# Optimization experiments

Hardware: AMD Instinct MI355X
Metric: run time of the kernel (lower is better)

Reference implementation:

```python
import jax, jax.numpy as jnp
import numpy as np

N = 50000      # ncount
IN_CH = 256    # in_channels
OUT_CH = 128   # out_channels
NNZ = 800000   # nnz per sparse matrix (avg degree 16)


def _spmm(rows, cols, vals, dense, n_rows):
    # sparse(COO) @ dense : gather rows of dense by col index, scale, scatter-add by row
    contrib = vals[:, None] * dense[cols]              # [nnz, F]
    return jax.ops.segment_sum(contrib, rows, num_segments=n_rows)


def setup_inputs() -> dict:
    key = jax.random.key(0)
    ks = jax.random.split(key, 12)
    phi_indices = jnp.stack([
        jax.random.randint(ks[0], (NNZ,), 0, N),
        jax.random.randint(ks[1], (NNZ,), 0, N)])
    phi_values = jax.random.normal(ks[2], (NNZ,), dtype=jnp.float32)
    phi_inverse_indices = jnp.stack([
        jax.random.randint(ks[3], (NNZ,), 0, N),
        jax.random.randint(ks[4], (NNZ,), 0, N)])
    phi_inverse_values = jax.random.normal(ks[5], (NNZ,), dtype=jnp.float32)
    feature_indices = jnp.stack([
        jax.random.randint(ks[6], (NNZ,), 0, N),       # node index
        jax.random.randint(ks[7], (NNZ,), 0, IN_CH)])  # feature column
    feature_values = jax.random.normal(ks[8], (NNZ,), dtype=jnp.float32)
    # xavier_uniform for weight_matrix
    limit = float(np.sqrt(6.0 / (IN_CH + OUT_CH)))
    weight_matrix = jax.random.uniform(ks[9], (IN_CH, OUT_CH), jnp.float32, -limit, limit)
    # diagonal filter Theta init uniform(0.9, 1.1)
    diagonal_weight_filter = jax.random.uniform(ks[10], (N,), jnp.float32, 0.9, 1.1)
    return {
        "phi_indices": phi_indices,
        "phi_values": phi_values,
        "phi_inverse_indices": phi_inverse_indices,
        "phi_inverse_values": phi_inverse_values,
        "feature_indices": feature_indices,
        "feature_values": feature_values,
        "weight_matrix": weight_matrix,
        "diagonal_weight_filter": diagonal_weight_filter,
        "dropout": 0,
    }


def reference(phi_indices, phi_values, phi_inverse_indices, phi_inverse_values,
              feature_indices, feature_values, weight_matrix,
              diagonal_weight_filter, dropout):
    # rescaled_phi = phi @ diag(theta): scales column j of phi by theta[j]
    scaled_phi_vals = phi_values * diagonal_weight_filter[phi_indices[1]]
    # filtered = features(sparse N x IN) @ W  -> [N, OUT]
    filtered = _spmm(feature_indices[0], feature_indices[1], feature_values,
                     weight_matrix, N)
    # (phi * D * phi_inv) @ filtered computed associatively without dense N x N:
    tmp = _spmm(phi_inverse_indices[0], phi_inverse_indices[1],
                phi_inverse_values, filtered, N)              # phi_inv @ filtered
    localized = _spmm(phi_indices[0], phi_indices[1],
                      scaled_phi_vals, tmp, N)                # (phi D) @ tmp
    # dropout in eval mode (training=False) is identity
    return jax.nn.relu(localized)
```

## Files before the change

### kernel.cpp

```cpp
#include <hip/hip_runtime.h>
#include <hip/hip_fp16.h>


#define OUT_CH 128
#define HALF_CH 64
#define RPB 256
#define RPB_SHIFT 8
#define MAX_NB 256
#define EPB 4096
#define EPT 16
#define MAX_CHUNK 16


__global__ __launch_bounds__(256) void bucket_hist_kernel(
    const int* __restrict__ rows0, int n0,
    const int* __restrict__ rows1, int n1,
    const int* __restrict__ rows2, int n2,
    int* __restrict__ hist_part,
    int NB, int NBLK)
{
    int m = blockIdx.y;
    const int* rows = (m == 0) ? rows0 : (m == 1) ? rows1 : rows2;
    int nnz         = (m == 0) ? n0    : (m == 1) ? n1    : n2;
    __shared__ int bins[MAX_NB];
    if (threadIdx.x < NB) bins[threadIdx.x] = 0;
    __syncthreads();
    int base = blockIdx.x * EPB;
    #pragma unroll 4
    for (int k = 0; k < EPB / 256; ++k) {
        int i = base + k * 256 + threadIdx.x;
        if (i < nnz) atomicAdd(&bins[rows[i] >> RPB_SHIFT], 1);
    }
    __syncthreads();
    int* out = hist_part + ((size_t)(m * NBLK + blockIdx.x)) * NB;
    if (threadIdx.x < NB) out[threadIdx.x] = bins[threadIdx.x];
}


__global__ __launch_bounds__(256) void scan_blocks_wave_kernel(
    int* __restrict__ hist_part, int* __restrict__ totals, int NB, int NBLK)
{
    int w = blockIdx.x * 4 + (threadIdx.x >> 6);
    if (w >= 3 * NB) return;
    int lane = threadIdx.x & 63;
    int m = w / NB, b = w - m * NB;
    const int chunk = (NBLK + 63) >> 6;
    int base_blk = lane * chunk;

    int v[MAX_CHUNK];
    int sum = 0;
    for (int k = 0; k < chunk; ++k) {
        int blk = base_blk + k;
        int x = (blk < NBLK) ? hist_part[((size_t)(m * NBLK + blk)) * NB + b] : 0;
        v[k] = x; sum += x;
    }
    int incl = sum;
    #pragma unroll
    for (int s = 1; s < 64; s <<= 1) {
        int y = __shfl_up(incl, s);
        if (lane >= s) incl += y;
    }
    int run = incl - sum;
    for (int k = 0; k < chunk; ++k) {
        int blk = base_blk + k;
        if (blk < NBLK) {
            hist_part[((size_t)(m * NBLK + blk)) * NB + b] = run;
            run += v[k];
        }
    }
    if (lane == 63) totals[w] = incl;
}


__global__ __launch_bounds__(1024) void scan_buckets_kernel(
    const int* __restrict__ totals, int* __restrict__ bases, int NB)
{
    int m = blockIdx.x;
    int t = threadIdx.x;
    int x = (t < NB) ? totals[m * NB + t] : 0;
    int lane = t & 63, wid = t >> 6;
    int incl = x;
    #pragma unroll
    for (int s = 1; s < 64; s <<= 1) {
        int y = __shfl_up(incl, s);
        if (lane >= s) incl += y;
    }
    __shared__ int wtot[16];
    __shared__ int wbase[16];
    if (lane == 63) wtot[wid] = incl;
    __syncthreads();
    if (t == 0) {
        int run = 0;
        #pragma unroll
        for (int w = 0; w < 16; ++w) { int v = wtot[w]; wbase[w] = run; run += v; }
    }
    __syncthreads();
    if (t < NB) bases[m * NB + t] = wbase[wid] + incl - x;
}


__global__ __launch_bounds__(256) void bucket_scatter_kernel(
    const int* __restrict__ rows0, const int* __restrict__ cols0, const float* __restrict__ vals0, int n0,
    const int* __restrict__ rows1, const int* __restrict__ cols1, const float* __restrict__ vals1, int n1,
    const int* __restrict__ rows2, const int* __restrict__ cols2, const float* __restrict__ vals2, int n2,
    const float* __restrict__ theta,
    const int* __restrict__ hist_part, const int* __restrict__ bases,
    int2* __restrict__ eb0, int2* __restrict__ eb1, int2* __restrict__ eb2,
    int NB, int NBLK)
{
    int m = blockIdx.y;
    const int* rows; const int* cols; const float* vals; int nnz; int2* eb;
    if (m == 0)      { rows = rows0; cols = cols0; vals = vals0; nnz = n0; eb = eb0; }
    else if (m == 1) { rows = rows1; cols = cols1; vals = vals1; nnz = n1; eb = eb1; }
    else             { rows = rows2; cols = cols2; vals = vals2; nnz = n2; eb = eb2; }

    __shared__ int2 staged[EPB];
    __shared__ unsigned char bucket_of[EPB];
    __shared__ int lhist[MAX_NB];
    __shared__ int lstart[MAX_NB + 1];
    __shared__ int lcur[MAX_NB];
    __shared__ int gbase[MAX_NB];
    __shared__ int wtot[4], wbase[4];

    int t = threadIdx.x;
    if (t < NB) lhist[t] = 0;
    __syncthreads();

    int base = blockIdx.x * EPB;
    bool fold = (m == 2);

    int  bk[EPT];
    int2 pl[EPT];
    #pragma unroll
    for (int k = 0; k < EPT; ++k) {
        int i = base + k * 256 + t;
        if (i < nnz) {
            int r = rows[i], c = cols[i];
            float v = vals[i];
            if (fold) v *= theta[c];
            bk[k] = r >> RPB_SHIFT;
            pl[k] = make_int2(c | ((r & (RPB - 1)) << 16), __float_as_int(v));
            atomicAdd(&lhist[bk[k]], 1);
        } else bk[k] = -1;
    }
    __syncthreads();

    {
        int x = (t < NB) ? lhist[t] : 0;
        int lane = t & 63, wid = t >> 6;
        int incl = x;
        #pragma unroll
        for (int s = 1; s < 64; s <<= 1) {
            int y = __shfl_up(incl, s);
            if (lane >= s) incl += y;
        }
        if (lane == 63) wtot[wid] = incl;
        __syncthreads();
        if (t == 0) {
            int run = 0;
            #pragma unroll
            for (int w = 0; w < 4; ++w) { int v = wtot[w]; wbase[w] = run; run += v; }
            lstart[MAX_NB] = run;
        }
        __syncthreads();
        if (t < NB) {
            int excl = wbase[wid] + incl - x;
            lstart[t] = excl;
            lcur[t]   = excl;
            const int* hp = hist_part + ((size_t)(m * NBLK + blockIdx.x)) * NB;
            gbase[t] = bases[m * NB + t] + hp[t];
        }
    }
    __syncthreads();

    #pragma unroll
    for (int k = 0; k < EPT; ++k) {
        if (bk[k] >= 0) {
            int idx = atomicAdd(&lcur[bk[k]], 1);
            staged[idx] = pl[k];
            bucket_of[idx] = (unsigned char)bk[k];
        }
    }
    __syncthreads();

    int count = min(EPB, nnz - base);
    for (int i = t; i < count; i += 256) {
        int b = bucket_of[i];
        int dest = gbase[b] + (i - lstart[b]);
        eb[dest] = staged[i];
    }
}


__global__ __launch_bounds__(256) void bucket_to_csr_kernel(
    const int2* __restrict__ eb0, const int2* __restrict__ eb1, const int2* __restrict__ eb2,
    int2* __restrict__ ec0, int2* __restrict__ ec1, int2* __restrict__ ec2,
    const int* __restrict__ bases,
    int* __restrict__ off,
    int n0, int n1, int n2, int NB, int n)
{
    int m = blockIdx.y;
    int b = blockIdx.x;
    const int2* eb; int2* ec; int nnz;
    if (m == 0)      { eb = eb0; ec = ec0; nnz = n0; }
    else if (m == 1) { eb = eb1; ec = ec1; nnz = n1; }
    else             { eb = eb2; ec = ec2; nnz = n2; }
    int base = bases[m * NB + b];
    int end  = (b + 1 < NB) ? bases[m * NB + b + 1] : nnz;

    __shared__ int hist[RPB];
    __shared__ int cur[RPB];
    __shared__ int loc[RPB + 1];
    __shared__ int wtot[4];
    __shared__ int wbase[4];
    int t = threadIdx.x;
    hist[t] = 0; cur[t] = 0;
    __syncthreads();
    for (int i = base + t; i < end; i += 256)
        atomicAdd(&hist[(eb[i].x >> 16) & (RPB - 1)], 1);
    __syncthreads();
    {
        int x = hist[t];
        int lane = t & 63, wid = t >> 6;
        int incl = x;
        #pragma unroll
        for (int s = 1; s < 64; s <<= 1) {
            int y = __shfl_up(incl, s);
            if (lane >= s) incl += y;
        }
        if (lane == 63) wtot[wid] = incl;
        __syncthreads();
        if (t == 0) {
            int run = 0;
            #pragma unroll
            for (int w = 0; w < 4; ++w) { int v = wtot[w]; wbase[w] = run; run += v; }
        }
        __syncthreads();
        loc[t] = wbase[wid] + incl - x;
        if (t == RPB - 1) loc[RPB] = wbase[3] + incl;
    }
    __syncthreads();
    {
        int r = b * RPB + t;
        if (r <= n) off[(size_t)m * (n + 1) + r] = base + loc[t];
        if (b == NB - 1 && t == 0) off[(size_t)m * (n + 1) + n] = nnz;
    }
    for (int i = base + t; i < end; i += 256) {
        int2 e = eb[i];
        int rl = (e.x >> 16) & (RPB - 1);
        int rk = atomicAdd(&cur[rl], 1);
        ec[base + loc[rl] + rk] = make_int2(e.x & 0xFFFF, e.y);
    }
}


template<bool SRC_H, bool DST_H, bool RELU>
__global__ __launch_bounds__(256) void spmm_csr_kernel(
    const int* __restrict__ off, const int2* __restrict__ edges,
    const void* __restrict__ dense_v, void* __restrict__ out_v, int nrows)
{
    int lane = threadIdx.x & 63;
    int r = blockIdx.x * 4 + (threadIdx.x >> 6);
    if (r >= nrows) return;
    int j   = __builtin_amdgcn_readfirstlane(off[r]);
    int end = __builtin_amdgcn_readfirstlane(off[r + 1]);
    const float2*  df = (const float2*)dense_v;
    const __half2* dh = (const __half2*)dense_v;

    float2 a0 = make_float2(0.f, 0.f), a1 = make_float2(0.f, 0.f);

    for (; j + 8 <= end; j += 8) {
        int2 e[8]; float2 d[8];
        #pragma unroll
        for (int k = 0; k < 8; ++k) e[k] = edges[j + k];
        #pragma unroll
        for (int k = 0; k < 8; ++k) {
            if (SRC_H) d[k] = __half22float2(dh[(size_t)e[k].x * HALF_CH + lane]);
            else       d[k] = df[(size_t)e[k].x * HALF_CH + lane];
        }
        #pragma unroll
        for (int k = 0; k < 8; ++k) {
            float v = __int_as_float(e[k].y);
            if (k & 1) { a1.x = fmaf(v, d[k].x, a1.x); a1.y = fmaf(v, d[k].y, a1.y); }
            else       { a0.x = fmaf(v, d[k].x, a0.x); a0.y = fmaf(v, d[k].y, a0.y); }
        }
    }
    for (; j + 4 <= end; j += 4) {
        int2 e[4]; float2 d[4];
        #pragma unroll
        for (int k = 0; k < 4; ++k) e[k] = edges[j + k];
        #pragma unroll
        for (int k = 0; k < 4; ++k) {
            if (SRC_H) d[k] = __half22float2(dh[(size_t)e[k].x * HALF_CH + lane]);
            else       d[k] = df[(size_t)e[k].x * HALF_CH + lane];
        }
        #pragma unroll
        for (int k = 0; k < 4; ++k) {
            float v = __int_as_float(e[k].y);
            if (k & 1) { a1.x = fmaf(v, d[k].x, a1.x); a1.y = fmaf(v, d[k].y, a1.y); }
            else       { a0.x = fmaf(v, d[k].x, a0.x); a0.y = fmaf(v, d[k].y, a0.y); }
        }
    }
    for (; j < end; ++j) {
        int2 e0 = edges[j];
        float2 d0;
        if (SRC_H) d0 = __half22float2(dh[(size_t)e0.x * HALF_CH + lane]);
        else       d0 = df[(size_t)e0.x * HALF_CH + lane];
        float v0 = __int_as_float(e0.y);
        a0.x = fmaf(v0, d0.x, a0.x); a0.y = fmaf(v0, d0.y, a0.y);
    }
    float2 res = make_float2(a0.x + a1.x, a0.y + a1.y);
    if (RELU) { res.x = fmaxf(res.x, 0.f); res.y = fmaxf(res.y, 0.f); }
    if (DST_H) ((__half2*)out_v)[(size_t)r * HALF_CH + lane] = __float22half2_rn(res);
    else       ((float2*) out_v)[(size_t)r * HALF_CH + lane] = res;
}


__global__ __launch_bounds__(256) void spmm_atomic_kernel(
    const int* __restrict__ rows, const int* __restrict__ cols,
    const float* __restrict__ vals, const float* __restrict__ theta,
    const float* __restrict__ dense, float* __restrict__ out, int nnz)
{
    int idx = blockIdx.x * blockDim.x + threadIdx.x;
    int e = idx >> 7;
    int f = idx & (OUT_CH - 1);
    if (e >= nnz) return;
    int r = rows[e];
    int c = cols[e];
    float v = vals[e];
    if (theta != nullptr) v *= theta[c];
    atomicAdd(&out[(size_t)r * OUT_CH + f], v * dense[(size_t)c * OUT_CH + f]);
}

__global__ __launch_bounds__(256) void relu_kernel(float* __restrict__ out, int n4)
{
    int i = blockIdx.x * blockDim.x + threadIdx.x;
    if (i >= n4) return;
    float4 v = ((float4*)out)[i];
    v.x = fmaxf(v.x, 0.f); v.y = fmaxf(v.y, 0.f);
    v.z = fmaxf(v.z, 0.f); v.w = fmaxf(v.w, 0.f);
    ((float4*)out)[i] = v;
}


static inline size_t align16(size_t x) { return (x + 15) & ~(size_t)15; }

extern "C" void kernel_launch(void* const* d_in, const int* in_sizes, int n_in,
                              void* d_out, int out_size, void* d_ws, size_t ws_size,
                              hipStream_t stream)
{
    const int*   phi_idx   = (const int*)d_in[0];
    const float* phi_vals  = (const float*)d_in[1];
    const int*   phii_idx  = (const int*)d_in[2];
    const float* phii_vals = (const float*)d_in[3];
    const int*   feat_idx  = (const int*)d_in[4];
    const float* feat_vals = (const float*)d_in[5];
    const float* W         = (const float*)d_in[6];
    const float* theta     = (const float*)d_in[7];

    const int nnz_phi  = in_sizes[1];
    const int nnz_phii = in_sizes[3];
    const int nnz_feat = in_sizes[5];
    const int n_nodes  = in_sizes[7];
    const int in_ch    = in_sizes[6] / OUT_CH;
    const size_t dense_elems = (size_t)n_nodes * OUT_CH;
    const long long total_e = (long long)nnz_feat + nnz_phii + nnz_phi;

    const int NB = (n_nodes + RPB - 1) >> RPB_SHIFT;
    int max_nnz = nnz_feat > nnz_phii ? nnz_feat : nnz_phii;
    if (nnz_phi > max_nnz) max_nnz = nnz_phi;
    const int NBLK = (max_nnz + EPB - 1) / EPB;

    size_t p = 0;
    size_t filtered_off = p; p += align16(dense_elems * sizeof(__half));
    size_t tmp_off      = p; p += align16(dense_elems * sizeof(__half));
    size_t off_off      = p; p += align16((size_t)3 * (n_nodes + 1) * sizeof(int));
    size_t hp_off       = p; p += align16((size_t)3 * NBLK * NB * sizeof(int));
    size_t tot_off      = p; p += align16((size_t)3 * NB * sizeof(int));
    size_t bas_off      = p; p += align16((size_t)3 * NB * sizeof(int));
    size_t eb_off       = p; p += align16((size_t)total_e * sizeof(int2));
    size_t ec_off       = p; p += align16((size_t)total_e * sizeof(int2));
    size_t need = p;

    char* ws = (char*)d_ws;
    dim3 block(256);

    bool fast_ok = (ws_size >= need) && (NB <= MAX_NB) && (n_nodes <= 65536) &&
                   (in_ch <= 65536) && (NBLK <= 64 * MAX_CHUNK);

    if (fast_ok) {
        __half* filtered = (__half*)(ws + filtered_off);
        __half* tmp      = (__half*)(ws + tmp_off);
        int* off_arr    = (int*)(ws + off_off);
        int* hist_part  = (int*)(ws + hp_off);
        int* totals     = (int*)(ws + tot_off);
        int* bases      = (int*)(ws + bas_off);
        int2* eb0 = (int2*)(ws + eb_off);
        int2* eb1 = eb0 + nnz_feat;
        int2* eb2 = eb1 + nnz_phii;
        int2* ec0 = (int2*)(ws + ec_off);
        int2* ec1 = ec0 + nnz_feat;
        int2* ec2 = ec1 + nnz_phii;

        const int* rows0 = feat_idx;  const int* cols0 = feat_idx + nnz_feat;
        const int* rows1 = phii_idx;  const int* cols1 = phii_idx + nnz_phii;
        const int* rows2 = phi_idx;   const int* cols2 = phi_idx  + nnz_phi;

        bucket_hist_kernel<<<dim3(NBLK, 3), block, 0, stream>>>(
            rows0, nnz_feat, rows1, nnz_phii, rows2, nnz_phi,
            hist_part, NB, NBLK);

        int nwaves = 3 * NB;
        scan_blocks_wave_kernel<<<dim3((nwaves + 3) / 4), block, 0, stream>>>(
            hist_part, totals, NB, NBLK);

        scan_buckets_kernel<<<dim3(3), dim3(1024), 0, stream>>>(totals, bases, NB);

        bucket_scatter_kernel<<<dim3(NBLK, 3), block, 0, stream>>>(
            rows0, cols0, feat_vals, nnz_feat,
            rows1, cols1, phii_vals, nnz_phii,
            rows2, cols2, phi_vals,  nnz_phi,
            theta, hist_part, bases, eb0, eb1, eb2, NB, NBLK);

        bucket_to_csr_kernel<<<dim3(NB, 3), block, 0, stream>>>(
            eb0, eb1, eb2, ec0, ec1, ec2, bases, off_arr,
            nnz_feat, nnz_phii, nnz_phi, NB, n_nodes);

        int* off_f  = off_arr;
        int* off_pi = off_arr + (n_nodes + 1);
        int* off_p  = off_arr + 2 * (n_nodes + 1);

        dim3 grid_r((unsigned)((n_nodes + 3) / 4));
        spmm_csr_kernel<false, true, false><<<grid_r, block, 0, stream>>>(
            off_f,  ec0, (const void*)W, (void*)filtered, n_nodes);
        spmm_csr_kernel<true, true, false><<<grid_r, block, 0, stream>>>(
            off_pi, ec1, (const void*)filtered, (void*)tmp, n_nodes);
        spmm_csr_kernel<true, false, true><<<grid_r, block, 0, stream>>>(
            off_p,  ec2, (const void*)tmp, d_out, n_nodes);
    } else {
        float* filtered = (float*)ws;
        float* tmp      = filtered + dense_elems;
        hipMemsetAsync(filtered, 0, 2 * dense_elems * sizeof(float), stream);
        hipMemsetAsync(d_out, 0, (size_t)out_size * sizeof(float), stream);
        {
            long long t = (long long)nnz_feat * OUT_CH;
            spmm_atomic_kernel<<<dim3((unsigned)((t + 255) / 256)), block, 0, stream>>>(
                feat_idx, feat_idx + nnz_feat, feat_vals, nullptr, W, filtered, nnz_feat);
        }
        {
            long long t = (long long)nnz_phii * OUT_CH;
            spmm_atomic_kernel<<<dim3((unsigned)((t + 255) / 256)), block, 0, stream>>>(
                phii_idx, phii_idx + nnz_phii, phii_vals, nullptr, filtered, tmp, nnz_phii);
        }
        {
            long long t = (long long)nnz_phi * OUT_CH;
            spmm_atomic_kernel<<<dim3((unsigned)((t + 255) / 256)), block, 0, stream>>>(
                phi_idx, phi_idx + nnz_phi, phi_vals, theta, tmp, (float*)d_out, nnz_phi);
        }
        {
            int n4 = out_size / 4;
            relu_kernel<<<dim3((n4 + 255) / 256), block, 0, stream>>>((float*)d_out, n4);
        }
    }
}
```

Measured before the change: 228.1 us.

## Pack CSR edges into 32-bit col+fp16 value and stage CSR writes in LDS

Each CSR edge is now packed as a 16-bit column index plus an fp16 value in one 32-bit word, replacing the int2 pair. This halves the edge bytes written by the CSR build and read by the three SpMM passes. The CSR kernel also stages its permuted output in shared memory when a bucket fits, so global writes become contiguous. The cost is a rounding of the sparse values to fp16, which lowers accuracy, and a larger shared-memory footprint that may reduce occupancy of the CSR build kernel.

```diff
diff --git a/kernel.cpp b/kernel.cpp
--- a/kernel.cpp
+++ b/kernel.cpp
@@ -10,6 +10,7 @@
 #define EPB 4096
 #define EPT 16
 #define MAX_CHUNK 16
+#define STAGE_CAP 8192
 
 
 __global__ __launch_bounds__(256) void bucket_hist_kernel(
@@ -194,20 +195,22 @@
 
 __global__ __launch_bounds__(256) void bucket_to_csr_kernel(
     const int2* __restrict__ eb0, const int2* __restrict__ eb1, const int2* __restrict__ eb2,
-    int2* __restrict__ ec0, int2* __restrict__ ec1, int2* __restrict__ ec2,
+    unsigned int* __restrict__ ec0, unsigned int* __restrict__ ec1, unsigned int* __restrict__ ec2,
     const int* __restrict__ bases,
     int* __restrict__ off,
     int n0, int n1, int n2, int NB, int n)
 {
     int m = blockIdx.y;
     int b = blockIdx.x;
-    const int2* eb; int2* ec; int nnz;
+    const int2* eb; unsigned int* ec; int nnz;
     if (m == 0)      { eb = eb0; ec = ec0; nnz = n0; }
     else if (m == 1) { eb = eb1; ec = ec1; nnz = n1; }
     else             { eb = eb2; ec = ec2; nnz = n2; }
     int base = bases[m * NB + b];
     int end  = (b + 1 < NB) ? bases[m * NB + b + 1] : nnz;
-
+    int cnt  = end - base;
+
+    __shared__ unsigned int staged_c[STAGE_CAP];
     __shared__ int hist[RPB];
     __shared__ int cur[RPB];
     __shared__ int loc[RPB + 1];
@@ -245,18 +248,32 @@
         if (r <= n) off[(size_t)m * (n + 1) + r] = base + loc[t];
         if (b == NB - 1 && t == 0) off[(size_t)m * (n + 1) + n] = nnz;
     }
-    for (int i = base + t; i < end; i += 256) {
-        int2 e = eb[i];
-        int rl = (e.x >> 16) & (RPB - 1);
-        int rk = atomicAdd(&cur[rl], 1);
-        ec[base + loc[rl] + rk] = make_int2(e.x & 0xFFFF, e.y);
+    if (cnt <= STAGE_CAP) {
+        for (int i = base + t; i < end; i += 256) {
+            int2 e = eb[i];
+            int rl = (e.x >> 16) & (RPB - 1);
+            int rk = atomicAdd(&cur[rl], 1);
+            unsigned short h = __half_as_ushort(__float2half_rn(__int_as_float(e.y)));
+            staged_c[loc[rl] + rk] = (unsigned int)(e.x & 0xFFFF) | ((unsigned int)h << 16);
+        }
+        __syncthreads();
+        for (int i = t; i < cnt; i += 256)
+            ec[base + i] = staged_c[i];
+    } else {
+        for (int i = base + t; i < end; i += 256) {
+            int2 e = eb[i];
+            int rl = (e.x >> 16) & (RPB - 1);
+            int rk = atomicAdd(&cur[rl], 1);
+            unsigned short h = __half_as_ushort(__float2half_rn(__int_as_float(e.y)));
+            ec[base + loc[rl] + rk] = (unsigned int)(e.x & 0xFFFF) | ((unsigned int)h << 16);
+        }
     }
 }
 
 
 template<bool SRC_H, bool DST_H, bool RELU>
 __global__ __launch_bounds__(256) void spmm_csr_kernel(
-    const int* __restrict__ off, const int2* __restrict__ edges,
+    const int* __restrict__ off, const unsigned int* __restrict__ edges,
     const void* __restrict__ dense_v, void* __restrict__ out_v, int nrows)
 {
     int lane = threadIdx.x & 63;
@@ -270,43 +287,43 @@
     float2 a0 = make_float2(0.f, 0.f), a1 = make_float2(0.f, 0.f);
 
     for (; j + 8 <= end; j += 8) {
-        int2 e[8]; float2 d[8];
+        unsigned int e[8]; float2 d[8];
         #pragma unroll
         for (int k = 0; k < 8; ++k) e[k] = edges[j + k];
         #pragma unroll
         for (int k = 0; k < 8; ++k) {
-            if (SRC_H) d[k] = __half22float2(dh[(size_t)e[k].x * HALF_CH + lane]);
-            else       d[k] = df[(size_t)e[k].x * HALF_CH + lane];
+            if (SRC_H) d[k] = __half22float2(dh[(size_t)(e[k] & 0xFFFF) * HALF_CH + lane]);
+            else       d[k] = df[(size_t)(e[k] & 0xFFFF) * HALF_CH + lane];
         }
         #pragma unroll
         for (int k = 0; k < 8; ++k) {
-            float v = __int_as_float(e[k].y);
+            float v = __half2float(__ushort_as_half((unsigned short)(e[k] >> 16)));
             if (k & 1) { a1.x = fmaf(v, d[k].x, a1.x); a1.y = fmaf(v, d[k].y, a1.y); }
             else       { a0.x = fmaf(v, d[k].x, a0.x); a0.y = fmaf(v, d[k].y, a0.y); }
         }
     }
     for (; j + 4 <= end; j += 4) {
-        int2 e[4]; float2 d[4];
+        unsigned int e[4]; float2 d[4];
         #pragma unroll
         for (int k = 0; k < 4; ++k) e[k] = edges[j + k];
         #pragma unroll
         for (int k = 0; k < 4; ++k) {
-            if (SRC_H) d[k] = __half22float2(dh[(size_t)e[k].x * HALF_CH + lane]);
-            else       d[k] = df[(size_t)e[k].x * HALF_CH + lane];
+            if (SRC_H) d[k] = __half22float2(dh[(size_t)(e[k] & 0xFFFF) * HALF_CH + lane]);
+            else       d[k] = df[(size_t)(e[k] & 0xFFFF) * HALF_CH + lane];
         }
         #pragma unroll
         for (int k = 0; k < 4; ++k) {
-            float v = __int_as_float(e[k].y);
+            float v = __half2float(__ushort_as_half((unsigned short)(e[k] >> 16)));
             if (k & 1) { a1.x = fmaf(v, d[k].x, a1.x); a1.y = fmaf(v, d[k].y, a1.y); }
             else       { a0.x = fmaf(v, d[k].x, a0.x); a0.y = fmaf(v, d[k].y, a0.y); }
         }
     }
     for (; j < end; ++j) {
-        int2 e0 = edges[j];
+        unsigned int e0 = edges[j];
         float2 d0;
-        if (SRC_H) d0 = __half22float2(dh[(size_t)e0.x * HALF_CH + lane]);
-        else       d0 = df[(size_t)e0.x * HALF_CH + lane];
-        float v0 = __int_as_float(e0.y);
+        if (SRC_H) d0 = __half22float2(dh[(size_t)(e0 & 0xFFFF) * HALF_CH + lane]);
+        else       d0 = df[(size_t)(e0 & 0xFFFF) * HALF_CH + lane];
+        float v0 = __half2float(__ushort_as_half((unsigned short)(e0 >> 16)));
         a0.x = fmaf(v0, d0.x, a0.x); a0.y = fmaf(v0, d0.y, a0.y);
     }
     float2 res = make_float2(a0.x + a1.x, a0.y + a1.y);
@@ -379,7 +396,7 @@
     size_t tot_off      = p; p += align16((size_t)3 * NB * sizeof(int));
     size_t bas_off      = p; p += align16((size_t)3 * NB * sizeof(int));
     size_t eb_off       = p; p += align16((size_t)total_e * sizeof(int2));
-    size_t ec_off       = p; p += align16((size_t)total_e * sizeof(int2));
+    size_t ec_off       = p; p += align16((size_t)total_e * sizeof(unsigned int));
     size_t need = p;
 
     char* ws = (char*)d_ws;
@@ -398,9 +415,9 @@
         int2* eb0 = (int2*)(ws + eb_off);
         int2* eb1 = eb0 + nnz_feat;
         int2* eb2 = eb1 + nnz_phii;
-        int2* ec0 = (int2*)(ws + ec_off);
-        int2* ec1 = ec0 + nnz_feat;
-        int2* ec2 = ec1 + nnz_phii;
+        unsigned int* ec0 = (unsigned int*)(ws + ec_off);
+        unsigned int* ec1 = ec0 + nnz_feat;
+        unsigned int* ec2 = ec1 + nnz_phii;
 
         const int* rows0 = feat_idx;  const int* cols0 = feat_idx + nnz_feat;
         const int* rows1 = phii_idx;  const int* cols1 = phii_idx + nnz_phii;
```

Measured after the change: 218.6 us (median of 2 runs). 1.04x faster.
